# Kernel optimization log

Measured on AMD Instinct MI355X. Metric: run time of the kernel, lower is better.

## Reference

```python
import jax, jax.numpy as jnp
import numpy as np


def setup_inputs() -> dict:
    key = jax.random.key(0)
    k1, k2 = jax.random.split(key)
    B, H, S, Dh = 2, 16, 2048, 64
    x1 = jax.random.normal(k1, (B, H, S, S), dtype=jnp.float32)   # attention scores
    x2 = jax.random.normal(k2, (B, H, Dh, S), dtype=jnp.float32)  # will be transposed to [B,H,S,Dh]
    return {"x1": x1, "x2": x2}


def reference(x1, x2):
    # F.softmax(x1, dim=-1).matmul(x2.transpose(-2, -1))
    # The Masker/sparsify in the original forward only packs activations for the
    # approximate backward pass; it does not change the forward output.
    sm = jax.nn.softmax(x1, axis=-1)                      # [B,H,Sq,Sk]
    out = jnp.einsum('bhqk,bhdk->bhqd', sm, x2)           # sm @ x2^T -> [B,H,Sq,Dh]
    return out
```

## Files before the change

### kernel.cpp

```cpp
#include <hip/hip_runtime.h>
#include <math.h>

typedef _Float16 f16x8 __attribute__((ext_vector_type(8)));
typedef float    f32x4 __attribute__((ext_vector_type(4)));

#define SEQ   2048
#define DH    64
#define BM    64
#define BK    64
#define PITCH 72
#define LOG2E 1.44269504088896340736f

extern "C" __global__ __launch_bounds__(256, 4)
void softmax_matmul_f16(const float* __restrict__ x1,
                        const float* __restrict__ x2,
                        float* __restrict__ out)
{
    __shared__ _Float16 ldsb[2][BM * PITCH];

    const int tid  = threadIdx.x;
    const int wave = tid >> 6;
    const int lane = tid & 63;
    const int r    = lane & 15;
    const int quad = lane >> 4;

    const int bh   = blockIdx.x >> 5;
    const int qblk = blockIdx.x & 31;
    const int row0 = qblk * BM + wave * 16;

    const float* x1row = x1 + ((size_t)bh * SEQ + (size_t)(row0 + r)) * SEQ;
    const float* x2bh  = x2 + (size_t)bh * DH * SEQ;
    float*       obase = out + ((size_t)bh * SEQ + (size_t)row0) * DH;

    const int sr = tid >> 2;
    const int sc = (tid & 3) * 16;
    const float* x2st = x2bh + (size_t)sr * SEQ + sc;
    _Float16* const ldsw0 = &ldsb[0][sr * PITCH + sc];
    _Float16* const ldsw1 = &ldsb[1][sr * PITCH + sc];

    f32x4 acc[4];
#pragma unroll
    for (int t = 0; t < 4; ++t) acc[t] = (f32x4){0.f, 0.f, 0.f, 0.f};

    float m = -INFINITY;
    float l = 0.0f;

    {
        float4 s0 = *(const float4*)(x2st + 0);
        float4 s1 = *(const float4*)(x2st + 4);
        float4 s2 = *(const float4*)(x2st + 8);
        float4 s3 = *(const float4*)(x2st + 12);
        f16x8 h0, h1;
        h0[0] = (_Float16)s0.x; h0[1] = (_Float16)s0.y; h0[2] = (_Float16)s0.z; h0[3] = (_Float16)s0.w;
        h0[4] = (_Float16)s1.x; h0[5] = (_Float16)s1.y; h0[6] = (_Float16)s1.z; h0[7] = (_Float16)s1.w;
        h1[0] = (_Float16)s2.x; h1[1] = (_Float16)s2.y; h1[2] = (_Float16)s2.z; h1[3] = (_Float16)s2.w;
        h1[4] = (_Float16)s3.x; h1[5] = (_Float16)s3.y; h1[6] = (_Float16)s3.z; h1[7] = (_Float16)s3.w;
        *(f16x8*)(ldsw0 + 0) = h0;
        *(f16x8*)(ldsw0 + 8) = h1;
    }

    const float* pf = x1row + quad * 8;
    float4 n0 = *(const float4*)(pf + 0);
    float4 n1 = *(const float4*)(pf + 4);
    float4 n2 = *(const float4*)(pf + 32);
    float4 n3 = *(const float4*)(pf + 36);

    __syncthreads();

    auto step = [&](int k0, const _Float16* __restrict__ rbase,
                    _Float16* __restrict__ wptr) {
        float xv[16];
        xv[0]  = n0.x; xv[1]  = n0.y; xv[2]  = n0.z; xv[3]  = n0.w;
        xv[4]  = n1.x; xv[5]  = n1.y; xv[6]  = n1.z; xv[7]  = n1.w;
        xv[8]  = n2.x; xv[9]  = n2.y; xv[10] = n2.z; xv[11] = n2.w;
        xv[12] = n3.x; xv[13] = n3.y; xv[14] = n3.z; xv[15] = n3.w;

        const int k1 = k0 + BK;
        const bool more = (k1 < SEQ);
        float4 s0, s1, s2, s3;
        if (more) {
            const float* pn = x1row + k1 + quad * 8;
            n0 = *(const float4*)(pn + 0);
            n1 = *(const float4*)(pn + 4);
            n2 = *(const float4*)(pn + 32);
            n3 = *(const float4*)(pn + 36);
            const float* ps = x2st + k1;
            s0 = *(const float4*)(ps + 0);
            s1 = *(const float4*)(ps + 4);
            s2 = *(const float4*)(ps + 8);
            s3 = *(const float4*)(ps + 12);
        }

        float a0 = fmaxf(xv[0], xv[1]),  a1 = fmaxf(xv[2], xv[3]);
        float a2 = fmaxf(xv[4], xv[5]),  a3 = fmaxf(xv[6], xv[7]);
        float a4 = fmaxf(xv[8], xv[9]),  a5 = fmaxf(xv[10], xv[11]);
        float a6 = fmaxf(xv[12], xv[13]), a7 = fmaxf(xv[14], xv[15]);
        float b0 = fmaxf(a0, a1), b1 = fmaxf(a2, a3);
        float b2 = fmaxf(a4, a5), b3 = fmaxf(a6, a7);
        float cmax = fmaxf(fmaxf(b0, b1), fmaxf(b2, b3));
        cmax = fmaxf(cmax, __shfl_xor(cmax, 16));
        cmax = fmaxf(cmax, __shfl_xor(cmax, 32));

        const float mnew  = fmaxf(m, cmax);
        const float alpha = __builtin_amdgcn_exp2f((m - mnew) * LOG2E);
        const float sh    = mnew * LOG2E;

        float p[16];
#pragma unroll
        for (int j = 0; j < 16; ++j)
            p[j] = __builtin_amdgcn_exp2f(__builtin_fmaf(xv[j], LOG2E, -sh));

        float c0 = p[0] + p[1],   c1 = p[2] + p[3];
        float c2 = p[4] + p[5],   c3 = p[6] + p[7];
        float c4 = p[8] + p[9],   c5 = p[10] + p[11];
        float c6 = p[12] + p[13], c7 = p[14] + p[15];
        float d0 = c0 + c1, d1 = c2 + c3, d2 = c4 + c5, d3 = c6 + c7;
        float rsum = (d0 + d1) + (d2 + d3);
        rsum += __shfl_xor(rsum, 16);
        rsum += __shfl_xor(rsum, 32);
        l = l * alpha + rsum;
        m = mnew;

        float ar[4];
#pragma unroll
        for (int g = 0; g < 4; ++g) ar[g] = __shfl(alpha, quad * 4 + g);
#pragma unroll
        for (int t = 0; t < 4; ++t)
#pragma unroll
            for (int g = 0; g < 4; ++g) acc[t][g] *= ar[g];

        f16x8 ah0, ah1;
#pragma unroll
        for (int j = 0; j < 8; ++j) {
            ah0[j] = (_Float16)p[j];
            ah1[j] = (_Float16)p[8 + j];
        }

#pragma unroll
        for (int t = 0; t < 4; ++t) {
            const _Float16* bp = rbase + (t * 16 + r) * PITCH + quad * 8;
            f16x8 bf0 = *(const f16x8*)(bp);
            f16x8 bf1 = *(const f16x8*)(bp + 32);
            acc[t] = __builtin_amdgcn_mfma_f32_16x16x32_f16(ah0, bf0, acc[t], 0, 0, 0);
            acc[t] = __builtin_amdgcn_mfma_f32_16x16x32_f16(ah1, bf1, acc[t], 0, 0, 0);
        }

        if (more) {
            f16x8 h0, h1;
            h0[0] = (_Float16)s0.x; h0[1] = (_Float16)s0.y; h0[2] = (_Float16)s0.z; h0[3] = (_Float16)s0.w;
            h0[4] = (_Float16)s1.x; h0[5] = (_Float16)s1.y; h0[6] = (_Float16)s1.z; h0[7] = (_Float16)s1.w;
            h1[0] = (_Float16)s2.x; h1[1] = (_Float16)s2.y; h1[2] = (_Float16)s2.z; h1[3] = (_Float16)s2.w;
            h1[4] = (_Float16)s3.x; h1[5] = (_Float16)s3.y; h1[6] = (_Float16)s3.z; h1[7] = (_Float16)s3.w;
            *(f16x8*)(wptr + 0) = h0;
            *(f16x8*)(wptr + 8) = h1;
        }
        __syncthreads();
    };

#pragma unroll 1
    for (int k0 = 0; k0 < SEQ; k0 += 2 * BK) {
        step(k0,      &ldsb[0][0], ldsw1);
        step(k0 + BK, &ldsb[1][0], ldsw0);
    }

    const float rl = 1.0f / l;
    float rlr[4];
#pragma unroll
    for (int g = 0; g < 4; ++g) rlr[g] = __shfl(rl, quad * 4 + g);
#pragma unroll
    for (int t = 0; t < 4; ++t)
#pragma unroll
        for (int g = 0; g < 4; ++g)
            obase[(size_t)(quad * 4 + g) * DH + t * 16 + r] = acc[t][g] * rlr[g];
}

extern "C" void kernel_launch(void* const* d_in, const int* in_sizes, int n_in,
                              void* d_out, int out_size, void* d_ws, size_t ws_size,
                              hipStream_t stream)
{
    const float* x1 = (const float*)d_in[0];
    const float* x2 = (const float*)d_in[1];
    float* out = (float*)d_out;

    const int bhCount = in_sizes[1] / (DH * SEQ);
    dim3 grid(bhCount * (SEQ / BM));
    dim3 block(256);
    hipLaunchKernelGGL(softmax_matmul_f16, grid, block, 0, stream, x1, x2, out);
}
```

Before: 723.7 us.

## Precompute softmax row max and sum in a separate pass, drop online rescaling

Adds a first kernel that reads each score row once to compute its max and exp-sum, storing them temporarily in the output buffer. The main kernel reads these stats, so it no longer needs per-tile max reductions, alpha rescaling of the accumulators or running-sum shuffles. It also prefetches x1 two tiles ahead. In exchange the large score tensor is read from memory twice, and there is an extra launch.

```diff
diff --git a/kernel.cpp b/kernel.cpp
--- a/kernel.cpp
+++ b/kernel.cpp
@@ -11,6 +11,49 @@
 #define PITCH 72
 #define LOG2E 1.44269504088896340736f
 
+extern "C" __global__ __launch_bounds__(256, 8)
+void softmax_stats(const float* __restrict__ x1, float* __restrict__ out)
+{
+    const int tid  = threadIdx.x;
+    const int wave = tid >> 6;
+    const int lane = tid & 63;
+    const size_t row = (size_t)blockIdx.x * 4 + wave;
+    const float* rp = x1 + row * SEQ + lane * 4;
+
+    float4 v[8];
+#pragma unroll
+    for (int i = 0; i < 8; ++i) v[i] = *(const float4*)(rp + i * 256);
+
+    float4 m4 = v[0];
+#pragma unroll
+    for (int i = 1; i < 8; ++i) {
+        m4.x = fmaxf(m4.x, v[i].x); m4.y = fmaxf(m4.y, v[i].y);
+        m4.z = fmaxf(m4.z, v[i].z); m4.w = fmaxf(m4.w, v[i].w);
+    }
+    float m = fmaxf(fmaxf(m4.x, m4.y), fmaxf(m4.z, m4.w));
+#pragma unroll
+    for (int s = 1; s < 64; s <<= 1) m = fmaxf(m, __shfl_xor(m, s));
+
+    const float sh = m * LOG2E;
+    float4 s4 = {0.f, 0.f, 0.f, 0.f};
+#pragma unroll
+    for (int i = 0; i < 8; ++i) {
+        s4.x += __builtin_amdgcn_exp2f(__builtin_fmaf(v[i].x, LOG2E, -sh));
+        s4.y += __builtin_amdgcn_exp2f(__builtin_fmaf(v[i].y, LOG2E, -sh));
+        s4.z += __builtin_amdgcn_exp2f(__builtin_fmaf(v[i].z, LOG2E, -sh));
+        s4.w += __builtin_amdgcn_exp2f(__builtin_fmaf(v[i].w, LOG2E, -sh));
+    }
+    float l = (s4.x + s4.y) + (s4.z + s4.w);
+#pragma unroll
+    for (int s = 1; s < 64; s <<= 1) l += __shfl_xor(l, s);
+
+    if (lane == 0) {
+        float* o = out + row * DH;
+        o[0] = m;
+        o[1] = l;
+    }
+}
+
 extern "C" __global__ __launch_bounds__(256, 4)
 void softmax_matmul_f16(const float* __restrict__ x1,
                         const float* __restrict__ x2,
@@ -28,9 +71,16 @@
     const int qblk = blockIdx.x & 31;
     const int row0 = qblk * BM + wave * 16;
 
-    const float* x1row = x1 + ((size_t)bh * SEQ + (size_t)(row0 + r)) * SEQ;
+    const size_t rbase_g = (size_t)bh * SEQ + (size_t)row0;
+    const float* x1row = x1 + (rbase_g + r) * SEQ;
     const float* x2bh  = x2 + (size_t)bh * DH * SEQ;
-    float*       obase = out + ((size_t)bh * SEQ + (size_t)row0) * DH;
+    float*       obase = out + rbase_g * DH;
+
+    const float sh = out[(rbase_g + r) * DH] * LOG2E;
+    float rlr[4];
+#pragma unroll
+    for (int g = 0; g < 4; ++g)
+        rlr[g] = 1.0f / out[(rbase_g + quad * 4 + g) * DH + 1];
 
     const int sr = tid >> 2;
     const int sc = (tid & 3) * 16;
@@ -41,9 +91,6 @@
     f32x4 acc[4];
 #pragma unroll
     for (int t = 0; t < 4; ++t) acc[t] = (f32x4){0.f, 0.f, 0.f, 0.f};
-
-    float m = -INFINITY;
-    float l = 0.0f;
 
     {
         float4 s0 = *(const float4*)(x2st + 0);
@@ -60,30 +107,51 @@
     }
 
     const float* pf = x1row + quad * 8;
-    float4 n0 = *(const float4*)(pf + 0);
-    float4 n1 = *(const float4*)(pf + 4);
-    float4 n2 = *(const float4*)(pf + 32);
-    float4 n3 = *(const float4*)(pf + 36);
+    float4 A0 = *(const float4*)(pf + 0);
+    float4 A1 = *(const float4*)(pf + 4);
+    float4 A2 = *(const float4*)(pf + 32);
+    float4 A3 = *(const float4*)(pf + 36);
+    pf = x1row + BK + quad * 8;
+    float4 B0 = *(const float4*)(pf + 0);
+    float4 B1 = *(const float4*)(pf + 4);
+    float4 B2 = *(const float4*)(pf + 32);
+    float4 B3 = *(const float4*)(pf + 36);
 
     __syncthreads();
 
-    auto step = [&](int k0, const _Float16* __restrict__ rbase,
-                    _Float16* __restrict__ wptr) {
-        float xv[16];
-        xv[0]  = n0.x; xv[1]  = n0.y; xv[2]  = n0.z; xv[3]  = n0.w;
-        xv[4]  = n1.x; xv[5]  = n1.y; xv[6]  = n1.z; xv[7]  = n1.w;
-        xv[8]  = n2.x; xv[9]  = n2.y; xv[10] = n2.z; xv[11] = n2.w;
-        xv[12] = n3.x; xv[13] = n3.y; xv[14] = n3.z; xv[15] = n3.w;
+    auto step = [&](int k0, const _Float16* __restrict__ rdbase,
+                    _Float16* __restrict__ wptr,
+                    float4& c0, float4& c1, float4& c2, float4& c3) {
+        f16x8 ah0, ah1;
+        ah0[0] = (_Float16)__builtin_amdgcn_exp2f(__builtin_fmaf(c0.x, LOG2E, -sh));
+        ah0[1] = (_Float16)__builtin_amdgcn_exp2f(__builtin_fmaf(c0.y, LOG2E, -sh));
+        ah0[2] = (_Float16)__builtin_amdgcn_exp2f(__builtin_fmaf(c0.z, LOG2E, -sh));
+        ah0[3] = (_Float16)__builtin_amdgcn_exp2f(__builtin_fmaf(c0.w, LOG2E, -sh));
+        ah0[4] = (_Float16)__builtin_amdgcn_exp2f(__builtin_fmaf(c1.x, LOG2E, -sh));
+        ah0[5] = (_Float16)__builtin_amdgcn_exp2f(__builtin_fmaf(c1.y, LOG2E, -sh));
+        ah0[6] = (_Float16)__builtin_amdgcn_exp2f(__builtin_fmaf(c1.z, LOG2E, -sh));
+        ah0[7] = (_Float16)__builtin_amdgcn_exp2f(__builtin_fmaf(c1.w, LOG2E, -sh));
+        ah1[0] = (_Float16)__builtin_amdgcn_exp2f(__builtin_fmaf(c2.x, LOG2E, -sh));
+        ah1[1] = (_Float16)__builtin_amdgcn_exp2f(__builtin_fmaf(c2.y, LOG2E, -sh));
+        ah1[2] = (_Float16)__builtin_amdgcn_exp2f(__builtin_fmaf(c2.z, LOG2E, -sh));
+        ah1[3] = (_Float16)__builtin_amdgcn_exp2f(__builtin_fmaf(c2.w, LOG2E, -sh));
+        ah1[4] = (_Float16)__builtin_amdgcn_exp2f(__builtin_fmaf(c3.x, LOG2E, -sh));
+        ah1[5] = (_Float16)__builtin_amdgcn_exp2f(__builtin_fmaf(c3.y, LOG2E, -sh));
+        ah1[6] = (_Float16)__builtin_amdgcn_exp2f(__builtin_fmaf(c3.z, LOG2E, -sh));
+        ah1[7] = (_Float16)__builtin_amdgcn_exp2f(__builtin_fmaf(c3.w, LOG2E, -sh));
+
+        const int kpf = k0 + 2 * BK;
+        if (kpf < SEQ) {
+            const float* pn = x1row + kpf + quad * 8;
+            c0 = *(const float4*)(pn + 0);
+            c1 = *(const float4*)(pn + 4);
+            c2 = *(const float4*)(pn + 32);
+            c3 = *(const float4*)(pn + 36);
+        }
 
         const int k1 = k0 + BK;
-        const bool more = (k1 < SEQ);
         float4 s0, s1, s2, s3;
-        if (more) {
-            const float* pn = x1row + k1 + quad * 8;
-            n0 = *(const float4*)(pn + 0);
-            n1 = *(const float4*)(pn + 4);
-            n2 = *(const float4*)(pn + 32);
-            n3 = *(const float4*)(pn + 36);
+        if (k1 < SEQ) {
             const float* ps = x2st + k1;
             s0 = *(const float4*)(ps + 0);
             s1 = *(const float4*)(ps + 4);
@@ -91,61 +159,16 @@
             s3 = *(const float4*)(ps + 12);
         }
 
-        float a0 = fmaxf(xv[0], xv[1]),  a1 = fmaxf(xv[2], xv[3]);
-        float a2 = fmaxf(xv[4], xv[5]),  a3 = fmaxf(xv[6], xv[7]);
-        float a4 = fmaxf(xv[8], xv[9]),  a5 = fmaxf(xv[10], xv[11]);
-        float a6 = fmaxf(xv[12], xv[13]), a7 = fmaxf(xv[14], xv[15]);
-        float b0 = fmaxf(a0, a1), b1 = fmaxf(a2, a3);
-        float b2 = fmaxf(a4, a5), b3 = fmaxf(a6, a7);
-        float cmax = fmaxf(fmaxf(b0, b1), fmaxf(b2, b3));
-        cmax = fmaxf(cmax, __shfl_xor(cmax, 16));
-        cmax = fmaxf(cmax, __shfl_xor(cmax, 32));
-
-        const float mnew  = fmaxf(m, cmax);
-        const float alpha = __builtin_amdgcn_exp2f((m - mnew) * LOG2E);
-        const float sh    = mnew * LOG2E;
-
-        float p[16];
-#pragma unroll
-        for (int j = 0; j < 16; ++j)
-            p[j] = __builtin_amdgcn_exp2f(__builtin_fmaf(xv[j], LOG2E, -sh));
-
-        float c0 = p[0] + p[1],   c1 = p[2] + p[3];
-        float c2 = p[4] + p[5],   c3 = p[6] + p[7];
-        float c4 = p[8] + p[9],   c5 = p[10] + p[11];
-        float c6 = p[12] + p[13], c7 = p[14] + p[15];
-        float d0 = c0 + c1, d1 = c2 + c3, d2 = c4 + c5, d3 = c6 + c7;
-        float rsum = (d0 + d1) + (d2 + d3);
-        rsum += __shfl_xor(rsum, 16);
-        rsum += __shfl_xor(rsum, 32);
-        l = l * alpha + rsum;
-        m = mnew;
-
-        float ar[4];
-#pragma unroll
-        for (int g = 0; g < 4; ++g) ar[g] = __shfl(alpha, quad * 4 + g);
-#pragma unroll
-        for (int t = 0; t < 4; ++t)
-#pragma unroll
-            for (int g = 0; g < 4; ++g) acc[t][g] *= ar[g];
-
-        f16x8 ah0, ah1;
-#pragma unroll
-        for (int j = 0; j < 8; ++j) {
-            ah0[j] = (_Float16)p[j];
-            ah1[j] = (_Float16)p[8 + j];
-        }
-
 #pragma unroll
         for (int t = 0; t < 4; ++t) {
-            const _Float16* bp = rbase + (t * 16 + r) * PITCH + quad * 8;
+            const _Float16* bp = rdbase + (t * 16 + r) * PITCH + quad * 8;
             f16x8 bf0 = *(const f16x8*)(bp);
             f16x8 bf1 = *(const f16x8*)(bp + 32);
             acc[t] = __builtin_amdgcn_mfma_f32_16x16x32_f16(ah0, bf0, acc[t], 0, 0, 0);
             acc[t] = __builtin_amdgcn_mfma_f32_16x16x32_f16(ah1, bf1, acc[t], 0, 0, 0);
         }
 
-        if (more) {
+        if (k1 < SEQ) {
             f16x8 h0, h1;
             h0[0] = (_Float16)s0.x; h0[1] = (_Float16)s0.y; h0[2] = (_Float16)s0.z; h0[3] = (_Float16)s0.w;
             h0[4] = (_Float16)s1.x; h0[5] = (_Float16)s1.y; h0[6] = (_Float16)s1.z; h0[7] = (_Float16)s1.w;
@@ -159,14 +182,10 @@
 
 #pragma unroll 1
     for (int k0 = 0; k0 < SEQ; k0 += 2 * BK) {
-        step(k0,      &ldsb[0][0], ldsw1);
-        step(k0 + BK, &ldsb[1][0], ldsw0);
-    }
-
-    const float rl = 1.0f / l;
-    float rlr[4];
-#pragma unroll
-    for (int g = 0; g < 4; ++g) rlr[g] = __shfl(rl, quad * 4 + g);
+        step(k0,      &ldsb[0][0], ldsw1, A0, A1, A2, A3);
+        step(k0 + BK, &ldsb[1][0], ldsw0, B0, B1, B2, B3);
+    }
+
 #pragma unroll
     for (int t = 0; t < 4; ++t)
 #pragma unroll
@@ -183,7 +202,11 @@
     float* out = (float*)d_out;
 
     const int bhCount = in_sizes[1] / (DH * SEQ);
-    dim3 grid(bhCount * (SEQ / BM));
     dim3 block(256);
-    hipLaunchKernelGGL(softmax_matmul_f16, grid, block, 0, stream, x1, x2, out);
+
+    dim3 g1(bhCount * SEQ / 4);
+    hipLaunchKernelGGL(softmax_stats, g1, block, 0, stream, x1, out);
+
+    dim3 g2(bhCount * (SEQ / BM));
+    hipLaunchKernelGGL(softmax_matmul_f16, g2, block, 0, stream, x1, x2, out);
 }
```

Result: slower. 819.7 us (+13.3%).
